# Kernel tuning notes

Hardware: AMD Instinct MI355X
Metric: run time of the kernel (lower is better)

The kernel has to match this reference:

```python
import jax, jax.numpy as jnp
import numpy as np

N, E, G = 50000, 800000, 64
F_IN, H, R, C = 64, 64, 3, 10


def setup_inputs() -> dict:
    key = jax.random.key(0)
    ks = jax.random.split(key, 16)
    s = 0.1
    return dict(
        x=jax.random.normal(ks[0], (N, F_IN), jnp.float32),
        edge_index=jax.random.randint(ks[1], (2, E), 0, N, dtype=jnp.int32),
        edge_type=jax.random.randint(ks[2], (E,), 0, R, dtype=jnp.int32),
        graph_batch=jnp.sort(jax.random.randint(ks[3], (N,), 0, G, dtype=jnp.int32)),
        # FiLMConv params (per-relation lin: bias=False; per-relation film: bias=True)
        film_lin_W=jax.random.normal(ks[4], (R, F_IN, H), jnp.float32) * s,
        film_film_W=jax.random.normal(ks[5], (R, F_IN, 2 * H), jnp.float32) * s,
        film_film_b=jnp.zeros((R, 2 * H), jnp.float32),
        skip_W=jax.random.normal(ks[6], (F_IN, H), jnp.float32) * s,
        skip_film_W=jax.random.normal(ks[7], (F_IN, 2 * H), jnp.float32) * s,
        skip_film_b=jnp.zeros((2 * H,), jnp.float32),
        # GATConv params (heads=1, concat=True, lin bias=False, final bias=True)
        gat_W=jax.random.normal(ks[8], (F_IN, H), jnp.float32) * s,
        gat_att_src=jax.random.normal(ks[9], (H,), jnp.float32) * s,
        gat_att_dst=jax.random.normal(ks[10], (H,), jnp.float32) * s,
        gat_b=jnp.zeros((H,), jnp.float32),
        # classifier MLP
        lin_W=jax.random.normal(ks[11], (4 * H, H), jnp.float32) * s,
        lin_b=jnp.zeros((H,), jnp.float32),
        fc_W=jax.random.normal(ks[12], (H, C), jnp.float32) * s,
        fc_b=jnp.zeros((C,), jnp.float32),
    )


def _film_conv(x, edge_index, edge_type, lin_W, film_W, film_b,
               skip_W, skip_film_W, skip_film_b):
    # PyG FiLMConv, aggr='mean' per relation, act=relu.
    n, r, h = x.shape[0], lin_W.shape[0], skip_W.shape[1]
    src, dst = edge_index[0], edge_index[1]
    fs = x @ skip_film_W + skip_film_b                  # [N,2H]; split -> (beta, gamma)
    out = jax.nn.relu(fs[:, h:] * (x @ skip_W) + fs[:, :h])
    xr = jnp.einsum('nd,rdh->rnh', x, lin_W)            # [R,N,H]
    fm = jnp.einsum('nd,rdh->rnh', x, film_W) + film_b[:, None, :]  # [R,N,2H]
    beta, gamma = fm[..., :h], fm[..., h:]
    # each edge uses its own relation's lin/film params
    msg = jax.nn.relu(gamma[edge_type, dst] * xr[edge_type, src] + beta[edge_type, dst])  # [E,H]
    seg = dst * r + edge_type                            # per-(node,relation) mean
    cnt = jax.ops.segment_sum(jnp.ones_like(msg[:, 0]), seg, num_segments=n * r)
    denom = jnp.maximum(cnt[seg], 1.0)
    agg = jax.ops.segment_sum(msg / denom[:, None], dst, num_segments=n)
    return out + agg


def _gat_conv(x, edge_index, W, att_src, att_dst, b):
    # PyG GATConv, heads=1, negative_slope=0.2, add_self_loops=True.
    n = x.shape[0]
    xp = x @ W                                           # [N,H]
    loop = jnp.arange(n, dtype=edge_index.dtype)
    src = jnp.concatenate([edge_index[0], loop])
    dst = jnp.concatenate([edge_index[1], loop])
    e = jax.nn.leaky_relu((xp @ att_src)[src] + (xp @ att_dst)[dst], 0.2)  # [E+N]
    m = jax.ops.segment_max(e, dst, num_segments=n)
    alpha = jnp.exp(e - m[dst])
    denom = jax.ops.segment_sum(alpha, dst, num_segments=n)
    alpha = alpha / denom[dst]
    return jax.ops.segment_sum(alpha[:, None] * xp[src], dst, num_segments=n) + b


def reference(x, edge_index, edge_type, graph_batch,
              film_lin_W, film_film_W, film_film_b, skip_W, skip_film_W, skip_film_b,
              gat_W, gat_att_src, gat_att_dst, gat_b,
              lin_W, lin_b, fc_W, fc_b):
    out1 = jax.nn.relu(_film_conv(x, edge_index, edge_type, film_lin_W, film_film_W,
                                  film_film_b, skip_W, skip_film_W, skip_film_b))
    out2 = jax.nn.relu(_gat_conv(x, edge_index, gat_W, gat_att_src, gat_att_dst, gat_b))
    feats = jnp.concatenate([out1, out2], axis=-1)       # [N,2H]
    g = G
    cnt = jax.ops.segment_sum(jnp.ones_like(feats[:, 0]), graph_batch, num_segments=g)
    mx = jax.ops.segment_max(feats, graph_batch, num_segments=g)
    mx = jnp.where(cnt[:, None] > 0, mx, 0.0)
    mean = jax.ops.segment_sum(feats, graph_batch, num_segments=g) / jnp.maximum(cnt, 1.0)[:, None]
    pooled = jnp.concatenate([mx, mean], axis=-1)        # [G,4H]
    hidden = jax.nn.relu(pooled @ lin_W + lin_b)         # dropout = identity (eval)
    logits = hidden @ fc_W + fc_b
    return jax.nn.log_softmax(logits, axis=-1)
```

## Files before the change

kernel.cpp:

```cpp
#include <hip/hip_runtime.h>
#include <hip/hip_bf16.h>

#define NN 50000
#define EE 800000
#define GG 64
#define RR 3
#define CC 10
#define RPL 16

typedef __attribute__((ext_vector_type(8))) short bf16x8;
typedef __attribute__((ext_vector_type(4))) float f32x4;

__device__ inline float leaky02(float x) { return x > 0.f ? x : 0.2f * x; }

__device__ inline void atomicMaxFPos(float* addr, float v) {
  atomicMax((int*)addr, __float_as_int(v));
}

__device__ inline unsigned short f2bf(float f) {
  __hip_bfloat16 b = __float2bfloat16(f);
  return *reinterpret_cast<unsigned short*>(&b);
}
__device__ inline float bf2f(unsigned short u) {
  return __uint_as_float(((unsigned int)u) << 16);
}

__global__ void scat_k(const int* __restrict__ ei, const int* __restrict__ et,
                       int* __restrict__ fill4, int* __restrict__ sorted,
                       const float* __restrict__ skip_film_W,
                       const float* __restrict__ skip_W,
                       const float* __restrict__ film_lin_W,
                       const float* __restrict__ film_film_W,
                       const float* __restrict__ gat_W,
                       const float* __restrict__ skip_film_b,
                       const float* __restrict__ film_film_b,
                       unsigned short* __restrict__ Wt,
                       float* __restrict__ bias) {
  int b = blockIdx.x;
  if (b < 3125) {
    int e = b * 256 + threadIdx.x;
    int src = ei[e], dst = ei[EE + e], t = et[e];
    int slot = atomicAdd(&fill4[dst * 4 + t], 1);
    if (slot < 32) sorted[dst * 96 + t * 32 + slot] = src;
    return;
  }
  int idx = (b - 3125) * 256 + threadIdx.x;
  if (idx >= 832 * 64 + 832) return;
  if (idx >= 832 * 64) {
    int c = idx - 832 * 64;
    float bv = 0.f;
    if (c < 128) bv = skip_film_b[c];
    else if (c >= 384 && c < 768) bv = film_film_b[c - 384];
    bias[c] = bv;
    return;
  }
  int c = idx >> 6, k = idx & 63;
  float v;
  if (c < 128)      v = skip_film_W[k * 128 + c];
  else if (c < 192) v = skip_W[k * 64 + (c - 128)];
  else if (c < 384) { int cc = c - 192, r = cc >> 6, h = cc & 63;
                      v = film_lin_W[(r * 64 + k) * 64 + h]; }
  else if (c < 768) { int cc = c - 384, r = cc >> 7, j = cc & 127;
                      v = film_film_W[(r * 64 + k) * 128 + j]; }
  else              v = gat_W[k * 64 + (c - 768)];
  Wt[idx] = f2bf(v);
}

__global__ __launch_bounds__(256) void gemm_k(const float* __restrict__ X,
    const unsigned short* __restrict__ Wt, const float* __restrict__ bias,
    const float* __restrict__ att_src, const float* __restrict__ att_dst,
    unsigned short* __restrict__ XP, unsigned short* __restrict__ XR,
    unsigned short* __restrict__ Ybg,
    unsigned short* __restrict__ S0b, float* __restrict__ as_,
    float* __restrict__ ad_) {
  __shared__ __align__(16) unsigned short As[64][72];
  __shared__ __align__(16) unsigned short Bs[128][72];
  const int tid = threadIdx.x;
  const int row0 = blockIdx.x * 64;

  {
    int r = tid >> 2, c0 = (tid & 3) * 16;
    int gr = row0 + r;
    ushort4 o0 = {0,0,0,0}, o1 = {0,0,0,0}, o2 = {0,0,0,0}, o3 = {0,0,0,0};
    if (gr < NN) {
      const float4* p = reinterpret_cast<const float4*>(X + (size_t)gr * 64 + c0);
      float4 v0 = p[0], v1 = p[1], v2 = p[2], v3 = p[3];
      o0 = {f2bf(v0.x), f2bf(v0.y), f2bf(v0.z), f2bf(v0.w)};
      o1 = {f2bf(v1.x), f2bf(v1.y), f2bf(v1.z), f2bf(v1.w)};
      o2 = {f2bf(v2.x), f2bf(v2.y), f2bf(v2.z), f2bf(v2.w)};
      o3 = {f2bf(v3.x), f2bf(v3.y), f2bf(v3.z), f2bf(v3.w)};
    }
    *reinterpret_cast<ushort4*>(&As[r][c0])      = o0;
    *reinterpret_cast<ushort4*>(&As[r][c0 + 4])  = o1;
    *reinterpret_cast<ushort4*>(&As[r][c0 + 8])  = o2;
    *reinterpret_cast<ushort4*>(&As[r][c0 + 12]) = o3;
  }
  __syncthreads();

  const int w = tid >> 6, lane = tid & 63;
  const int m = lane & 15, q = lane >> 4;
  bf16x8 a0 = *reinterpret_cast<const bf16x8*>(&As[16 * w + m][q * 8]);
  bf16x8 a1 = *reinterpret_cast<const bf16x8*>(&As[16 * w + m][32 + q * 8]);
  const int rbase = row0 + 16 * w + q * 4;

  f32x4 t0[8], t1[4], t6[4];

  for (int tile = 0; tile < 7; tile++) {
    __syncthreads();
    int col0 = tile * 128;
    int width = (tile == 6) ? 64 : 128;
    {
      int c = tid >> 1, half = (tid & 1) * 32;
      if (c < width) {
        int gc = col0 + c;
        const uint4* p = reinterpret_cast<const uint4*>(Wt + (size_t)gc * 64 + half);
        uint4 v0 = p[0], v1 = p[1], v2 = p[2], v3 = p[3];
        *reinterpret_cast<uint4*>(&Bs[c][half])      = v0;
        *reinterpret_cast<uint4*>(&Bs[c][half + 8])  = v1;
        *reinterpret_cast<uint4*>(&Bs[c][half + 16]) = v2;
        *reinterpret_cast<uint4*>(&Bs[c][half + 24]) = v3;
      }
    }
    __syncthreads();
    #pragma unroll
    for (int ct = 0; ct < 8; ct++) {
      if (tile == 6 && ct >= 4) continue;
      bf16x8 b0 = *reinterpret_cast<const bf16x8*>(&Bs[ct * 16 + m][q * 8]);
      bf16x8 b1 = *reinterpret_cast<const bf16x8*>(&Bs[ct * 16 + m][32 + q * 8]);
      f32x4 acc = {0.f, 0.f, 0.f, 0.f};
      acc = __builtin_amdgcn_mfma_f32_16x16x32_bf16(a0, b0, acc, 0, 0, 0);
      acc = __builtin_amdgcn_mfma_f32_16x16x32_bf16(a1, b1, acc, 0, 0, 0);
      if (tile == 0) { t0[ct] = acc; continue; }
      if (tile == 1 && ct < 4) { t1[ct] = acc; continue; }
      if (tile == 6) t6[ct] = acc;
      int colm = ct * 16 + m;
      float bv = (tile >= 3 && tile <= 5) ? bias[col0 + colm] : 0.f;
      #pragma unroll
      for (int rg = 0; rg < 4; rg++) {
        int gr = rbase + rg;
        if (gr >= NN) continue;
        float v = acc[rg];
        if (tile == 1) {
          XR[(size_t)gr * 64 + (colm - 64)] = f2bf(v);
        } else if (tile == 2) {
          if (ct < 4) XR[((size_t)NN + gr) * 64 + colm]            = f2bf(v);
          else        XR[((size_t)2 * NN + gr) * 64 + (colm - 64)] = f2bf(v);
        } else if (tile <= 5) {
          Ybg[(size_t)gr * 384 + (col0 - 384) + colm] = f2bf(v + bv);
        } else {
          XP[(size_t)gr * 64 + colm] = f2bf(v);
        }
      }
    }
  }

  float pa[4] = {0.f, 0.f, 0.f, 0.f}, pd[4] = {0.f, 0.f, 0.f, 0.f};
  #pragma unroll
  for (int j = 0; j < 4; j++) {
    int h = 16 * j + m;
    float bb = bias[h];
    float bg = bias[64 + h];
    float asv = att_src[h];
    float adv = att_dst[h];
    #pragma unroll
    for (int rg = 0; rg < 4; rg++) {
      float so = fmaxf((t0[4 + j][rg] + bg) * t1[j][rg] + (t0[j][rg] + bb), 0.f);
      int gr = rbase + rg;
      if (gr < NN) S0b[(size_t)gr * 64 + h] = f2bf(so);
      pa[rg] += t6[j][rg] * asv;
      pd[rg] += t6[j][rg] * adv;
    }
  }
  #pragma unroll
  for (int ofs = 1; ofs < 16; ofs <<= 1) {
    #pragma unroll
    for (int rg = 0; rg < 4; rg++) {
      pa[rg] += __shfl_xor(pa[rg], ofs);
      pd[rg] += __shfl_xor(pd[rg], ofs);
    }
  }
  if (m == 0) {
    #pragma unroll
    for (int rg = 0; rg < 4; rg++) {
      int gr = rbase + rg;
      if (gr < NN) { as_[gr] = pa[rg]; ad_[gr] = pd[rg]; }
    }
  }
}

#define RPN 16

__global__ __launch_bounds__(256) void dst_k(const int* __restrict__ sorted,
    const int* __restrict__ fill4, const unsigned short* __restrict__ XP,
    const unsigned short* __restrict__ XR,
    const unsigned short* __restrict__ Ybg,
    const unsigned short* __restrict__ S0b,
    const float* __restrict__ as_, const float* __restrict__ ad_,
    const float* __restrict__ gat_b, const int* __restrict__ gb,
    float* __restrict__ pmax, float* __restrict__ psum,
    int* __restrict__ gstart, int* __restrict__ gend) {
  __shared__ int   s_pk[4][96];
  __shared__ float s_w [4][96];
  __shared__ int   s_d [4][4];
  __shared__ int   s_g[4];
  __shared__ float s_ad[4];
  __shared__ __align__(16) unsigned short s_rows[64][128];
  float* s_val = (float*)&s_rows[0][0];

  const int tid = threadIdx.x;
  const int wid = tid >> 6, h = tid & 63;
  const int n0 = blockIdx.x * 4;
  const int n  = n0 + wid;

  size_t rep = (size_t)(blockIdx.x & (RPL - 1)) * GG * 128;
  pmax += rep; psum += rep;

  if (tid < 16) {
    int wd = tid >> 2, t = tid & 3;
    if (t < 3) {
      int d = fill4[(n0 + wd) * 4 + t];
      s_d[wd][t] = d > 32 ? 32 : d;
    } else {
      s_g[wd]  = gb[n0 + wd];
      s_ad[wd] = ad_[n0 + wd];
    }
  }
  __syncthreads();

  for (int i = tid; i < 512; i += 256) {
    int wd = i >> 7, s = i & 127;
    if (s < 96) {
      int tt = s >> 5, j = s & 31;
      if (j < s_d[wd][tt]) {
        int cidx = (tt == 0) ? j
                 : (tt == 1) ? s_d[wd][0] + j
                             : s_d[wd][0] + s_d[wd][1] + j;
        int src = sorted[(size_t)(n0 + wd) * 96 + s];
        s_pk[wd][cidx] = src;
        s_w[wd][cidx]  = leaky02(as_[src] + s_ad[wd]);
      }
    }
  }
  __syncthreads();

  const int d0 = s_d[wid][0], d1 = s_d[wid][1], d2 = s_d[wid][2];
  const int sB = d0 + d1;
  const int deg = sB + d2;
  const float adn = s_ad[wid];
  float es = leaky02(as_[n] + adn);

  bool v1 = h < deg;
  bool v2 = h + 64 < deg;
  float e1 = v1 ? s_w[wid][h]      : -1e30f;
  float e2 = v2 ? s_w[wid][64 + h] : -1e30f;
  float mg = fmaxf(fmaxf(e1, e2), es);
  #pragma unroll
  for (int ofs = 1; ofs < 64; ofs <<= 1) mg = fmaxf(mg, __shfl_xor(mg, ofs));
  float w1 = v1 ? __expf(e1 - mg) : 0.f;
  float w2 = v2 ? __expf(e2 - mg) : 0.f;
  if (v1) s_w[wid][h] = w1;
  if (v2) s_w[wid][64 + h] = w2;
  float den = w1 + w2;
  #pragma unroll
  for (int ofs = 1; ofs < 64; ofs <<= 1) den += __shfl_xor(den, ofs);
  float ws = __expf(es - mg);
  den += ws;

  const float i0 = 1.f / (float)(d0 > 1 ? d0 : 1);
  const float i1 = 1.f / (float)(d1 > 1 ? d1 : 1);
  const float i2 = 1.f / (float)(d2 > 1 ? d2 : 1);
  const unsigned short* ybg = Ybg + (size_t)n * 384;
  const float b0p = bf2f(ybg[h])       * i0, g0p = bf2f(ybg[64 + h])  * i0;
  const float b1p = bf2f(ybg[128 + h]) * i1, g1p = bf2f(ybg[192 + h]) * i1;
  const float b2p = bf2f(ybg[256 + h]) * i2, g2p = bf2f(ybg[320 + h]) * i2;

  float S = ws * bf2f(XP[(size_t)n * 64 + h]);
  float f = 0.f;

  const int grp16 = tid >> 4, lane16 = tid & 15;
  int kA[4], kB[4], kD[4];
  #pragma unroll
  for (int k = 0; k < 4; k++) {
    kA[k] = s_d[k][0];
    kB[k] = kA[k] + s_d[k][1];
    kD[k] = kB[k] + s_d[k][2];
  }
  int dmax = max(max(kD[0], kD[1]), max(kD[2], kD[3]));
  int rounds = (dmax + RPN - 1) / RPN;

  for (int r = 0; r < rounds; r++) {
    int e0 = r * RPN;
    #pragma unroll
    for (int k = 0; k < 4; k++) {
      int jj = e0 + grp16;
      if (jj < kD[k]) {
        int src = s_pk[k][jj];
        int t = jj < kA[k] ? 0 : (jj < kB[k] ? 1 : 2);
        const unsigned short* row = (lane16 < 8)
            ? XP + (size_t)src * 64 + lane16 * 8
            : XR + ((size_t)t * NN + src) * 64 + (lane16 - 8) * 8;
        uint4 v = *reinterpret_cast<const uint4*>(row);
        *reinterpret_cast<uint4*>(&s_rows[16 * k + grp16][lane16 * 8]) = v;
      }
    }
    __syncthreads();
    const unsigned short* rowp = &s_rows[wid * RPN][0];
    int hi0 = min(e0 + RPN, d0);
    for (int i = e0; i < hi0; i++) {
      float wj = s_w[wid][i];
      int sr = i - e0;
      float xp = bf2f(rowp[sr * 128 + h]);
      float xr = bf2f(rowp[sr * 128 + 64 + h]);
      S += wj * xp;
      f += fmaxf(g0p * xr + b0p, 0.f);
    }
    int lo1 = max(e0, d0), hi1 = min(e0 + RPN, sB);
    for (int i = lo1; i < hi1; i++) {
      float wj = s_w[wid][i];
      int sr = i - e0;
      float xp = bf2f(rowp[sr * 128 + h]);
      float xr = bf2f(rowp[sr * 128 + 64 + h]);
      S += wj * xp;
      f += fmaxf(g1p * xr + b1p, 0.f);
    }
    int lo2 = max(e0, sB), hi2 = min(e0 + RPN, deg);
    for (int i = lo2; i < hi2; i++) {
      float wj = s_w[wid][i];
      int sr = i - e0;
      float xp = bf2f(rowp[sr * 128 + h]);
      float xr = bf2f(rowp[sr * 128 + 64 + h]);
      S += wj * xp;
      f += fmaxf(g2p * xr + b2p, 0.f);
    }
    __syncthreads();
  }

  float o1 = fmaxf(bf2f(S0b[(size_t)n * 64 + h]) + f, 0.f);
  float o2 = fmaxf(S / den + gat_b[h], 0.f);

  s_val[wid * 128 + h]      = o1;
  s_val[wid * 128 + 64 + h] = o2;
  if (h == 0) {
    int g = s_g[wid];
    if (n == 0 || gb[n - 1] != g)      gstart[g] = n;
    if (n == NN - 1 || gb[n + 1] != g) gend[g] = n;
  }
  __syncthreads();
  if (tid < 128) {
    int fch = tid;
    int curg = s_g[0];
    float v0 = s_val[fch];
    float mx = v0, sm = v0;
    #pragma unroll
    for (int j = 1; j < 4; j++) {
      float v = s_val[j * 128 + fch];
      if (s_g[j] == curg) { mx = fmaxf(mx, v); sm += v; }
      else {
        atomicMaxFPos(&pmax[curg * 128 + fch], mx);
        atomicAdd(&psum[curg * 128 + fch], sm);
        curg = s_g[j]; mx = v; sm = v;
      }
    }
    atomicMaxFPos(&pmax[curg * 128 + fch], mx);
    atomicAdd(&psum[curg * 128 + fch], sm);
  }
}

__global__ __launch_bounds__(64) void head_k(const float* __restrict__ pmax,
    const float* __restrict__ psum, const int* __restrict__ gstart,
    const int* __restrict__ gend,
    const float* __restrict__ lin_W, const float* __restrict__ lin_b,
    const float* __restrict__ fc_W, const float* __restrict__ fc_b,
    float* __restrict__ out) {
  __shared__ float p[256];
  __shared__ float hid[64];
  __shared__ float lg[CC];
  __shared__ float lse;
  int g = blockIdx.x, t = threadIdx.x;
  int s = gstart[g], e = gend[g];
  int cnt = (s <= e && s < NN && s >= 0) ? (e - s + 1) : 0;
  float invc = 1.f / (float)(cnt > 1 ? cnt : 1);
  for (int i = t; i < 256; i += 64) {
    if (i < 128) {
      float mx = 0.f;
      for (int r = 0; r < RPL; r++)
        mx = fmaxf(mx, pmax[((size_t)r * GG + g) * 128 + i]);
      p[i] = mx;
    } else {
      int f = i - 128;
      float sm = 0.f;
      for (int r = 0; r < RPL; r++)
        sm += psum[((size_t)r * GG + g) * 128 + f];
      p[i] = sm * invc;
    }
  }
  __syncthreads();
  float acc = lin_b[t];
  for (int k = 0; k < 256; k++) acc += p[k] * lin_W[k * 64 + t];
  hid[t] = fmaxf(acc, 0.f);
  __syncthreads();
  if (t < CC) {
    float a = fc_b[t];
    for (int k = 0; k < 64; k++) a += hid[k] * fc_W[k * CC + t];
    lg[t] = a;
  }
  __syncthreads();
  if (t == 0) {
    float mx = lg[0];
    for (int i = 1; i < CC; i++) mx = fmaxf(mx, lg[i]);
    float sum = 0.f;
    for (int i = 0; i < CC; i++) sum += expf(lg[i] - mx);
    lse = mx + logf(sum);
  }
  __syncthreads();
  if (t < CC) out[g * CC + t] = lg[t] - lse;
}

extern "C" void kernel_launch(void* const* d_in, const int* in_sizes, int n_in,
                              void* d_out, int out_size, void* d_ws, size_t ws_size,
                              hipStream_t stream) {
  const float* x            = (const float*)d_in[0];
  const int*   edge_index   = (const int*)d_in[1];
  const int*   edge_type    = (const int*)d_in[2];
  const int*   graph_batch  = (const int*)d_in[3];
  const float* film_lin_W   = (const float*)d_in[4];
  const float* film_film_W  = (const float*)d_in[5];
  const float* film_film_b  = (const float*)d_in[6];
  const float* skip_W       = (const float*)d_in[7];
  const float* skip_film_W  = (const float*)d_in[8];
  const float* skip_film_b  = (const float*)d_in[9];
  const float* gat_W        = (const float*)d_in[10];
  const float* att_src      = (const float*)d_in[11];
  const float* att_dst      = (const float*)d_in[12];
  const float* gat_b        = (const float*)d_in[13];
  const float* lin_W        = (const float*)d_in[14];
  const float* lin_b        = (const float*)d_in[15];
  const float* fc_W         = (const float*)d_in[16];
  const float* fc_b         = (const float*)d_in[17];
  float* out                = (float*)d_out;

  float* ws = (float*)d_ws;
  const size_t N = NN, G = GG;
  size_t oXP     = 0;
  size_t oXR     = N * 32;
  size_t oYbg    = oXR + N * 96;
  size_t oS0     = oYbg + N * 192;
  size_t oAs     = oS0 + N * 32;
  size_t oAd     = oAs + N;
  size_t oWt     = oAd + N;
  size_t oBias   = oWt + 832 * 32;
  size_t oPmax   = oBias + 832;
  size_t oPsum   = oPmax + (size_t)RPL * G * 128;
  size_t oGend   = oPsum + (size_t)RPL * G * 128;
  size_t oFill   = oGend + G;
  size_t oGstart = oFill + N * 4;
  size_t oSorted = oGstart + G;

  unsigned short* XP  = (unsigned short*)(ws + oXP);
  unsigned short* XR  = (unsigned short*)(ws + oXR);
  unsigned short* Ybg = (unsigned short*)(ws + oYbg);
  unsigned short* S0b = (unsigned short*)(ws + oS0);
  float* as_    = ws + oAs;
  float* ad_    = ws + oAd;
  unsigned short* Wt  = (unsigned short*)(ws + oWt);
  float* bias   = ws + oBias;
  float* pmax   = ws + oPmax;
  float* psum   = ws + oPsum;
  int*   gend   = (int*)(ws + oGend);
  int*   fill4  = (int*)(ws + oFill);
  int*   gstart = (int*)(ws + oGstart);
  int*   sorted = (int*)(ws + oSorted);

  size_t zeroFloats = oGstart - oPmax;
  hipMemsetAsync(pmax, 0, zeroFloats * sizeof(float), stream);

  scat_k<<<3125 + 210, 256, 0, stream>>>(edge_index, edge_type, fill4, sorted,
      skip_film_W, skip_W, film_lin_W, film_film_W, gat_W,
      skip_film_b, film_film_b, Wt, bias);
  gemm_k<<<(NN + 63) / 64, 256, 0, stream>>>(x, Wt, bias, att_src, att_dst,
                                             XP, XR, Ybg, S0b, as_, ad_);
  dst_k<<<NN / 4, 256, 0, stream>>>(sorted, fill4, XP, XR, Ybg, S0b, as_, ad_,
                                    gat_b, graph_batch, pmax, psum,
                                    gstart, gend);
  head_k<<<GG, 64, 0, stream>>>(pmax, psum, gstart, gend,
                                lin_W, lin_b, fc_W, fc_b, out);
}
```

Measured before the change: 248.5 us.

## Overlap edge bucketing with node GEMM in one fused launch

```diff
diff --git a/kernel.cpp b/kernel.cpp
--- a/kernel.cpp
+++ b/kernel.cpp
@@ -7,6 +7,8 @@
 #define RR 3
 #define CC 10
 #define RPL 16
+#define NBG 782
+#define NBS 1563
 
 typedef __attribute__((ext_vector_type(8))) short bf16x8;
 typedef __attribute__((ext_vector_type(4))) float f32x4;
@@ -25,26 +27,16 @@
   return __uint_as_float(((unsigned int)u) << 16);
 }
 
-__global__ void scat_k(const int* __restrict__ ei, const int* __restrict__ et,
-                       int* __restrict__ fill4, int* __restrict__ sorted,
-                       const float* __restrict__ skip_film_W,
-                       const float* __restrict__ skip_W,
-                       const float* __restrict__ film_lin_W,
-                       const float* __restrict__ film_film_W,
-                       const float* __restrict__ gat_W,
-                       const float* __restrict__ skip_film_b,
-                       const float* __restrict__ film_film_b,
-                       unsigned short* __restrict__ Wt,
-                       float* __restrict__ bias) {
-  int b = blockIdx.x;
-  if (b < 3125) {
-    int e = b * 256 + threadIdx.x;
-    int src = ei[e], dst = ei[EE + e], t = et[e];
-    int slot = atomicAdd(&fill4[dst * 4 + t], 1);
-    if (slot < 32) sorted[dst * 96 + t * 32 + slot] = src;
-    return;
-  }
-  int idx = (b - 3125) * 256 + threadIdx.x;
+__global__ void wpack_k(const float* __restrict__ skip_film_W,
+                        const float* __restrict__ skip_W,
+                        const float* __restrict__ film_lin_W,
+                        const float* __restrict__ film_film_W,
+                        const float* __restrict__ gat_W,
+                        const float* __restrict__ skip_film_b,
+                        const float* __restrict__ film_film_b,
+                        unsigned short* __restrict__ Wt,
+                        float* __restrict__ bias) {
+  int idx = blockIdx.x * 256 + threadIdx.x;
   if (idx >= 832 * 64 + 832) return;
   if (idx >= 832 * 64) {
     int c = idx - 832 * 64;
@@ -66,18 +58,34 @@
   Wt[idx] = f2bf(v);
 }
 
-__global__ __launch_bounds__(256) void gemm_k(const float* __restrict__ X,
+__global__ __launch_bounds__(256) void fuse_k(const float* __restrict__ X,
     const unsigned short* __restrict__ Wt, const float* __restrict__ bias,
     const float* __restrict__ att_src, const float* __restrict__ att_dst,
     unsigned short* __restrict__ XP, unsigned short* __restrict__ XR,
     unsigned short* __restrict__ Ybg,
     unsigned short* __restrict__ S0b, float* __restrict__ as_,
-    float* __restrict__ ad_) {
+    float* __restrict__ ad_,
+    const int* __restrict__ ei, const int* __restrict__ et,
+    int* __restrict__ fill4, int* __restrict__ sorted) {
   __shared__ __align__(16) unsigned short As[64][72];
   __shared__ __align__(16) unsigned short Bs[128][72];
   const int tid = threadIdx.x;
+
+  if (blockIdx.x >= NBG) {
+    int e = (blockIdx.x - NBG) * 512 + tid * 2;
+    if (e < EE) {
+      int2 s2 = *reinterpret_cast<const int2*>(ei + e);
+      int2 d2 = *reinterpret_cast<const int2*>(ei + EE + e);
+      int2 t2 = *reinterpret_cast<const int2*>(et + e);
+      int slot = atomicAdd(&fill4[d2.x * 4 + t2.x], 1);
+      if (slot < 32) sorted[d2.x * 96 + t2.x * 32 + slot] = s2.x;
+      slot = atomicAdd(&fill4[d2.y * 4 + t2.y], 1);
+      if (slot < 32) sorted[d2.y * 96 + t2.y * 32 + slot] = s2.y;
+    }
+    return;
+  }
+
   const int row0 = blockIdx.x * 64;
-
   {
     int r = tid >> 2, c0 = (tid & 3) * 16;
     int gr = row0 + r;
@@ -474,11 +482,12 @@
   size_t zeroFloats = oGstart - oPmax;
   hipMemsetAsync(pmax, 0, zeroFloats * sizeof(float), stream);
 
-  scat_k<<<3125 + 210, 256, 0, stream>>>(edge_index, edge_type, fill4, sorted,
-      skip_film_W, skip_W, film_lin_W, film_film_W, gat_W,
-      skip_film_b, film_film_b, Wt, bias);
-  gemm_k<<<(NN + 63) / 64, 256, 0, stream>>>(x, Wt, bias, att_src, att_dst,
-                                             XP, XR, Ybg, S0b, as_, ad_);
+  wpack_k<<<212, 256, 0, stream>>>(skip_film_W, skip_W, film_lin_W,
+                                   film_film_W, gat_W, skip_film_b,
+                                   film_film_b, Wt, bias);
+  fuse_k<<<NBG + NBS, 256, 0, stream>>>(x, Wt, bias, att_src, att_dst,
+                                        XP, XR, Ybg, S0b, as_, ad_,
+                                        edge_index, edge_type, fill4, sorted);
   dst_k<<<NN / 4, 256, 0, stream>>>(sorted, fill4, XP, XR, Ybg, S0b, as_, ad_,
                                     gat_b, graph_batch, pmax, psum,
                                     gstart, gend);
```

Result: faster. 239.5 us (-3.6%).
